# Optimization experiments

Measured on AMD Instinct MI355X. Metric: run time of the kernel, lower is better.

The kernel has to match this reference:

```python
import jax, jax.numpy as jnp
import numpy as np

COMMITMENT_WEIGHT = 0.25


def setup_inputs() -> dict:
    key = jax.random.key(0)
    k1, k2 = jax.random.split(key)
    z = jax.random.normal(k1, (16, 512, 2048), dtype=jnp.float32)
    codebooks = jax.random.normal(k2, (8, 1024, 512), dtype=jnp.float32) * 0.01
    return {"z": z, "codebooks": codebooks}


def reference(z, codebooks):
    """Residual VQ forward (eval mode, no EMA update).
    z: [B, D, T], codebooks: [Q, N, D].
    Returns (quantized [B, D, T], codes [B, Q, T], total_loss scalar).
    """
    B, D, T = z.shape
    Q = codebooks.shape[0]
    zt = jnp.transpose(z, (0, 2, 1))  # [B, T, D]

    residual = zt
    quantized = jnp.zeros_like(zt)
    codes = []
    total_loss = jnp.float32(0.0)
    for q in range(Q):
        cb = codebooks[q]  # [N, D]
        # squared euclidean distances (argmin-equivalent to cdist)
        d2 = (jnp.sum(residual * residual, axis=-1, keepdims=True)
              - 2.0 * jnp.einsum('btd,nd->btn', residual, cb)
              + jnp.sum(cb * cb, axis=-1))  # [B, T, N]
        idx = jnp.argmin(d2, axis=-1)  # [B, T]
        codes.append(idx)
        q_step = cb[idx]  # [B, T, D] embedding gather
        quantized = quantized + q_step
        commit = jnp.mean((jax.lax.stop_gradient(residual) - q_step) ** 2)
        commit = jnp.clip(commit, 0.0, 10.0)
        total_loss = total_loss + commit * COMMITMENT_WEIGHT
        residual = residual - jax.lax.stop_gradient(q_step)

    total_loss = jnp.clip(total_loss, 0.0, 10.0)
    q_bdt = jnp.transpose(quantized, (0, 2, 1))  # [B, D, T]
    # faithful to original: raw reshape of [B,T,D] -> [B,D,T] (not a transpose)
    z_res = zt.reshape(B, D, T)
    out = z_res + jax.lax.stop_gradient(q_bdt - z_res)  # straight-through
    codes = jnp.stack(codes, axis=1)  # [B, Q, T]
    return out, codes, total_loss
```

## Files before the change

### kernel.cpp

```cpp
#include <hip/hip_runtime.h>
#include <cfloat>

#define BB 16
#define DD 512
#define TT 2048
#define QQ 8
#define NN 1024
#define MM 16
#define RS 520

__device__ __forceinline__ float np_block128_sq(const float* a) {
    float r[8];
    #pragma unroll
    for (int j = 0; j < 8; ++j) r[j] = __fmul_rn(a[j], a[j]);
    #pragma unroll
    for (int i = 8; i < 128; i += 8)
        #pragma unroll
        for (int j = 0; j < 8; ++j) r[j] = __fadd_rn(r[j], __fmul_rn(a[i + j], a[i + j]));
    return __fadd_rn(__fadd_rn(__fadd_rn(r[0], r[1]), __fadd_rn(r[2], r[3])),
                     __fadd_rn(__fadd_rn(r[4], r[5]), __fadd_rn(r[6], r[7])));
}
__device__ __forceinline__ float np_sum_sq_512(const float* p) {
    const float b0 = np_block128_sq(p);
    const float b1 = np_block128_sq(p + 128);
    const float b2 = np_block128_sq(p + 256);
    const float b3 = np_block128_sq(p + 384);
    return __fadd_rn(__fadd_rn(b0, b1), __fadd_rn(b2, b3));
}

__global__ __launch_bounds__(64) void rvq_init(double* lossws) {
    if (threadIdx.x < QQ) lossws[threadIdx.x] = 0.0;
}

__global__ __launch_bounds__(256) void rvq_cnorm(const float* __restrict__ cbs,
                                                 float* __restrict__ cnorm) {
    const int gid = blockIdx.x * 256 + threadIdx.x;
    cnorm[gid] = np_sum_sq_512(cbs + (size_t)gid * DD);
}

__global__ __launch_bounds__(256) void rvq_argmin(const float* __restrict__ z,
                                                  const float* __restrict__ cbs,
                                                  const float* __restrict__ cnorm,
                                                  int* __restrict__ codes_ws) {
    __shared__ float resid[MM * RS];
    __shared__ float A_sh[MM];
    __shared__ int   sel[MM];
    __shared__ float redv[MM * 128];
    __shared__ int   redi[MM * 128];

    const int tid = threadIdx.x;
    const int blk = blockIdx.x;
    const int b   = blk >> 7;
    const int t0  = (blk & 127) * MM;
    const float* zb = z + (size_t)b * DD * TT + t0;

    for (int p = 0; p < 32; ++p) {
        const int d = (tid >> 4) + p * 16;
        const int m = tid & 15;
        resid[m * RS + d] = zb[(size_t)d * TT + m];
    }
    __syncthreads();
    if (tid < MM) A_sh[tid] = np_sum_sq_512(resid + tid * RS);

    const int half  = tid >> 7;
    const int nl    = tid & 127;
    const int mbase = half * 8;

    for (int q = 0; q < QQ; ++q) {
        __syncthreads();
        const float* cbq = cbs + (size_t)q * NN * DD;

        float bv[8]; int bi[8];
        #pragma unroll
        for (int i = 0; i < 8; ++i) { bv[i] = FLT_MAX; bi[i] = 0; }

        for (int nb = 0; nb < 2; ++nb) {
            const int n0 = nb * 512 + nl;
            const float* c0 = cbq + (size_t)(n0      ) * DD;
            const float* c1 = cbq + (size_t)(n0 + 128) * DD;
            const float* c2 = cbq + (size_t)(n0 + 256) * DD;
            const float* c3 = cbq + (size_t)(n0 + 384) * DD;

            float4 acc[8][4];
            #pragma unroll
            for (int m = 0; m < 8; ++m)
                #pragma unroll
                for (int j = 0; j < 4; ++j) acc[m][j] = make_float4(0.f, 0.f, 0.f, 0.f);

            const float* rb = resid + mbase * RS;

            for (int k8 = 0; k8 < 64; ++k8) {
                const int ko = k8 * 8;
                const float4 w0a = *(const float4*)(c0 + ko), w0b = *(const float4*)(c0 + ko + 4);
                const float4 w1a = *(const float4*)(c1 + ko), w1b = *(const float4*)(c1 + ko + 4);
                const float4 w2a = *(const float4*)(c2 + ko), w2b = *(const float4*)(c2 + ko + 4);
                const float4 w3a = *(const float4*)(c3 + ko), w3b = *(const float4*)(c3 + ko + 4);
                #pragma unroll
                for (int m = 0; m < 8; ++m) {
                    const float4 r0 = *(const float4*)(rb + m * RS + ko);
                    const float4 r1 = *(const float4*)(rb + m * RS + ko + 4);
                    acc[m][0].x = __fadd_rn(acc[m][0].x, __fmul_rn(r0.x, w0a.x));
                    acc[m][0].y = __fadd_rn(acc[m][0].y, __fmul_rn(r0.y, w0a.y));
                    acc[m][0].z = __fadd_rn(acc[m][0].z, __fmul_rn(r0.z, w0a.z));
                    acc[m][0].w = __fadd_rn(acc[m][0].w, __fmul_rn(r0.w, w0a.w));
                    acc[m][0].x = __fadd_rn(acc[m][0].x, __fmul_rn(r1.x, w0b.x));
                    acc[m][0].y = __fadd_rn(acc[m][0].y, __fmul_rn(r1.y, w0b.y));
                    acc[m][0].z = __fadd_rn(acc[m][0].z, __fmul_rn(r1.z, w0b.z));
                    acc[m][0].w = __fadd_rn(acc[m][0].w, __fmul_rn(r1.w, w0b.w));
                    acc[m][1].x = __fadd_rn(acc[m][1].x, __fmul_rn(r0.x, w1a.x));
                    acc[m][1].y = __fadd_rn(acc[m][1].y, __fmul_rn(r0.y, w1a.y));
                    acc[m][1].z = __fadd_rn(acc[m][1].z, __fmul_rn(r0.z, w1a.z));
                    acc[m][1].w = __fadd_rn(acc[m][1].w, __fmul_rn(r0.w, w1a.w));
                    acc[m][1].x = __fadd_rn(acc[m][1].x, __fmul_rn(r1.x, w1b.x));
                    acc[m][1].y = __fadd_rn(acc[m][1].y, __fmul_rn(r1.y, w1b.y));
                    acc[m][1].z = __fadd_rn(acc[m][1].z, __fmul_rn(r1.z, w1b.z));
                    acc[m][1].w = __fadd_rn(acc[m][1].w, __fmul_rn(r1.w, w1b.w));
                    acc[m][2].x = __fadd_rn(acc[m][2].x, __fmul_rn(r0.x, w2a.x));
                    acc[m][2].y = __fadd_rn(acc[m][2].y, __fmul_rn(r0.y, w2a.y));
                    acc[m][2].z = __fadd_rn(acc[m][2].z, __fmul_rn(r0.z, w2a.z));
                    acc[m][2].w = __fadd_rn(acc[m][2].w, __fmul_rn(r0.w, w2a.w));
                    acc[m][2].x = __fadd_rn(acc[m][2].x, __fmul_rn(r1.x, w2b.x));
                    acc[m][2].y = __fadd_rn(acc[m][2].y, __fmul_rn(r1.y, w2b.y));
                    acc[m][2].z = __fadd_rn(acc[m][2].z, __fmul_rn(r1.z, w2b.z));
                    acc[m][2].w = __fadd_rn(acc[m][2].w, __fmul_rn(r1.w, w2b.w));
                    acc[m][3].x = __fadd_rn(acc[m][3].x, __fmul_rn(r0.x, w3a.x));
                    acc[m][3].y = __fadd_rn(acc[m][3].y, __fmul_rn(r0.y, w3a.y));
                    acc[m][3].z = __fadd_rn(acc[m][3].z, __fmul_rn(r0.z, w3a.z));
                    acc[m][3].w = __fadd_rn(acc[m][3].w, __fmul_rn(r0.w, w3a.w));
                    acc[m][3].x = __fadd_rn(acc[m][3].x, __fmul_rn(r1.x, w3b.x));
                    acc[m][3].y = __fadd_rn(acc[m][3].y, __fmul_rn(r1.y, w3b.y));
                    acc[m][3].z = __fadd_rn(acc[m][3].z, __fmul_rn(r1.z, w3b.z));
                    acc[m][3].w = __fadd_rn(acc[m][3].w, __fmul_rn(r1.w, w3b.w));
                }
            }
            #pragma unroll
            for (int j = 0; j < 4; ++j) {
                const int n = n0 + j * 128;
                const float Cn = cnorm[q * NN + n];
                #pragma unroll
                for (int m = 0; m < 8; ++m) {
                    const float4 a = acc[m][j];
                    const float E = __fadd_rn(__fadd_rn(a.x, a.z), __fadd_rn(a.y, a.w));
                    const float s = __fadd_rn(__fsub_rn(A_sh[mbase + m], __fmul_rn(2.0f, E)), Cn);
                    if (s < bv[m]) { bv[m] = s; bi[m] = n; }
                }
            }
        }

        __syncthreads();
        #pragma unroll
        for (int m = 0; m < 8; ++m) {
            redv[(mbase + m) * 128 + nl] = bv[m];
            redi[(mbase + m) * 128 + nl] = bi[m];
        }
        __syncthreads();
        {
            const int m = tid >> 4, j0 = tid & 15;
            float v  = redv[m * 128 + j0];
            int   ix = redi[m * 128 + j0];
            for (int u = 1; u < 8; ++u) {
                const float v2 = redv[m * 128 + j0 + 16 * u];
                const int   i2 = redi[m * 128 + j0 + 16 * u];
                if (v2 < v || (v2 == v && i2 < ix)) { v = v2; ix = i2; }
            }
            #pragma unroll
            for (int mask = 1; mask < 16; mask <<= 1) {
                const float v2 = __shfl_xor(v, mask, 64);
                const int   i2 = __shfl_xor(ix, mask, 64);
                if (v2 < v || (v2 == v && i2 < ix)) { v = v2; ix = i2; }
            }
            if (j0 == 0) {
                sel[m] = ix;
                codes_ws[b * QQ * TT + q * TT + t0 + m] = ix;
            }
        }
        __syncthreads();

        if (q < QQ - 1) {
            const int m = tid >> 4, l16 = tid & 15;
            const float* cr = cbq + (size_t)sel[m] * DD;
            for (int jj = 0; jj < 32; ++jj) {
                const int d = l16 + jj * 16;
                resid[m * RS + d] = __fsub_rn(resid[m * RS + d], cr[d]);
            }
            __syncthreads();
            if (tid < MM) A_sh[tid] = np_sum_sq_512(resid + tid * RS);
        }
    }
}

__global__ __launch_bounds__(256) void rvq_build(const float* __restrict__ z,
                                                 const float* __restrict__ cbs,
                                                 const int* __restrict__ codes_ws,
                                                 float* __restrict__ out,
                                                 double* __restrict__ lossws) {
    __shared__ int    lcode[MM * QQ];
    __shared__ double lpart[4][QQ];

    const int tid = threadIdx.x;
    const int blk = blockIdx.x;
    const int b   = blk >> 7;
    const int t0  = (blk & 127) * MM;

    if (tid < MM * QQ) {
        const int m = tid >> 3;
        const int q = tid & 7;
        const int c = codes_ws[b * QQ * TT + q * TT + t0 + m];
        lcode[tid] = c;
        out[(size_t)BB * DD * TT + (size_t)b * QQ * TT + (size_t)q * TT + t0 + m] = (float)c;
    }
    __syncthreads();

    const int m  = tid & 15;
    const int dl = tid >> 4;

    double lsum[QQ];
    #pragma unroll
    for (int q = 0; q < QQ; ++q) lsum[q] = 0.0;

    for (int p = 0; p < DD / 16; ++p) {
        const int d = dl + p * 16;
        float r  = z[(size_t)b * DD * TT + (size_t)d * TT + t0 + m];
        float qa = 0.0f;
        #pragma unroll
        for (int q = 0; q < QQ; ++q) {
            const float c = cbs[(size_t)q * NN * DD + (size_t)lcode[m * 8 + q] * DD + d];
            qa = __fadd_rn(qa, c);
            r  = __fsub_rn(r, c);
            lsum[q] += (double)r * (double)r;
        }
        out[(size_t)b * DD * TT + (size_t)d * TT + t0 + m] = qa;
    }

    const int wid = tid >> 6, lane = tid & 63;
    #pragma unroll
    for (int q = 0; q < QQ; ++q) {
        double v = lsum[q];
        #pragma unroll
        for (int off = 32; off > 0; off >>= 1) v += __shfl_down(v, off, 64);
        lsum[q] = v;
    }
    if (lane == 0) {
        #pragma unroll
        for (int q = 0; q < QQ; ++q) lpart[wid][q] = lsum[q];
    }
    __syncthreads();
    if (tid < QQ) {
        const double s = lpart[0][tid] + lpart[1][tid] + lpart[2][tid] + lpart[3][tid];
        atomicAdd(&lossws[tid], s);
    }
}

__global__ __launch_bounds__(64) void rvq_final(const double* __restrict__ lossws,
                                                float* __restrict__ out) {
    if (threadIdx.x == 0) {
        double tot = 0.0;
        for (int q = 0; q < QQ; ++q) {
            double c = lossws[q] / (double)((size_t)BB * TT * DD);
            c = c < 0.0 ? 0.0 : (c > 10.0 ? 10.0 : c);
            tot += 0.25 * c;
        }
        tot = tot < 0.0 ? 0.0 : (tot > 10.0 ? 10.0 : tot);
        out[(size_t)BB * DD * TT + (size_t)BB * QQ * TT] = (float)tot;
    }
}

extern "C" void kernel_launch(void* const* d_in, const int* in_sizes, int n_in,
                              void* d_out, int out_size, void* d_ws, size_t ws_size,
                              hipStream_t stream) {
    const float* z   = (const float*)d_in[0];
    const float* cbs = (const float*)d_in[1];
    float* out       = (float*)d_out;
    double* lossws   = (double*)d_ws;
    float* cnorm     = (float*)((char*)d_ws + 64);
    int* codes_ws    = (int*)((char*)d_ws + 64 + QQ * NN * 4);

    rvq_init  <<<1, 64, 0, stream>>>(lossws);
    rvq_cnorm <<<QQ * NN / 256, 256, 0, stream>>>(cbs, cnorm);
    rvq_argmin<<<BB * (TT / MM), 256, 0, stream>>>(z, cbs, cnorm, codes_ws);
    rvq_build <<<BB * (TT / MM), 256, 0, stream>>>(z, cbs, codes_ws, out, lossws);
    rvq_final <<<1, 64, 0, stream>>>(lossws, out);
}
```

Baseline: 8.717 ms.

## Use FMA-contracted distance pass with exact rescoring of near-minimum candidates

The main codebook-distance loop now uses plain multiply-adds the compiler may fuse into FMAs, instead of separate correctly-rounded multiply and add. Each thread keeps its top-two candidates, and the block finds the approximate minimum per row. Candidates within a small margin are then rescored with the original strict arithmetic, and the winner is picked with a packed 64-bit atomicMin. The accumulator tile is halved and launch bounds now request 4 blocks, to cut register pressure and raise occupancy. The risk is that the margin may miss the true argmin when FMA rounding moves a score by more than that margin, and the rescoring adds serial per-thread dot products.

```diff
diff --git a/kernel.cpp b/kernel.cpp
--- a/kernel.cpp
+++ b/kernel.cpp
@@ -8,6 +8,7 @@
 #define NN 1024
 #define MM 16
 #define RS 520
+#define MARGIN 1e-3f
 
 __device__ __forceinline__ float np_block128_sq(const float* a) {
     float r[8];
@@ -27,6 +28,20 @@
     const float b3 = np_block128_sq(p + 384);
     return __fadd_rn(__fadd_rn(b0, b1), __fadd_rn(b2, b3));
 }
+__device__ __forceinline__ float np_dot_512(const float* r, const float* w) {
+    float a0 = 0.f, a1 = 0.f, a2 = 0.f, a3 = 0.f;
+    for (int ko = 0; ko < 512; ko += 8) {
+        a0 = __fadd_rn(a0, __fmul_rn(r[ko + 0], w[ko + 0]));
+        a1 = __fadd_rn(a1, __fmul_rn(r[ko + 1], w[ko + 1]));
+        a2 = __fadd_rn(a2, __fmul_rn(r[ko + 2], w[ko + 2]));
+        a3 = __fadd_rn(a3, __fmul_rn(r[ko + 3], w[ko + 3]));
+        a0 = __fadd_rn(a0, __fmul_rn(r[ko + 4], w[ko + 4]));
+        a1 = __fadd_rn(a1, __fmul_rn(r[ko + 5], w[ko + 5]));
+        a2 = __fadd_rn(a2, __fmul_rn(r[ko + 6], w[ko + 6]));
+        a3 = __fadd_rn(a3, __fmul_rn(r[ko + 7], w[ko + 7]));
+    }
+    return __fadd_rn(__fadd_rn(a0, a2), __fadd_rn(a1, a3));
+}
 
 __global__ __launch_bounds__(64) void rvq_init(double* lossws) {
     if (threadIdx.x < QQ) lossws[threadIdx.x] = 0.0;
@@ -38,15 +53,16 @@
     cnorm[gid] = np_sum_sq_512(cbs + (size_t)gid * DD);
 }
 
-__global__ __launch_bounds__(256) void rvq_argmin(const float* __restrict__ z,
-                                                  const float* __restrict__ cbs,
-                                                  const float* __restrict__ cnorm,
-                                                  int* __restrict__ codes_ws) {
+__global__ __launch_bounds__(256, 4) void rvq_argmin(const float* __restrict__ z,
+                                                     const float* __restrict__ cbs,
+                                                     const float* __restrict__ cnorm,
+                                                     int* __restrict__ codes_ws) {
     __shared__ float resid[MM * RS];
     __shared__ float A_sh[MM];
     __shared__ int   sel[MM];
-    __shared__ float redv[MM * 128];
-    __shared__ int   redi[MM * 128];
+    __shared__ float wmin[4][8];
+    __shared__ float amin_sh[MM];
+    __shared__ unsigned long long cand_sh[MM];
 
     const int tid = threadIdx.x;
     const int blk = blockIdx.x;
@@ -65,114 +81,122 @@
     const int half  = tid >> 7;
     const int nl    = tid & 127;
     const int mbase = half * 8;
+    const int wv    = tid >> 6;
+    const float* rb = resid + mbase * RS;
 
     for (int q = 0; q < QQ; ++q) {
         __syncthreads();
         const float* cbq = cbs + (size_t)q * NN * DD;
 
-        float bv[8]; int bi[8];
-        #pragma unroll
-        for (int i = 0; i < 8; ++i) { bv[i] = FLT_MAX; bi[i] = 0; }
-
-        for (int nb = 0; nb < 2; ++nb) {
-            const int n0 = nb * 512 + nl;
-            const float* c0 = cbq + (size_t)(n0      ) * DD;
-            const float* c1 = cbq + (size_t)(n0 + 128) * DD;
-            const float* c2 = cbq + (size_t)(n0 + 256) * DD;
-            const float* c3 = cbq + (size_t)(n0 + 384) * DD;
-
-            float4 acc[8][4];
+        float Af[8];
+        #pragma unroll
+        for (int mm = 0; mm < 8; ++mm) Af[mm] = A_sh[mbase + mm];
+
+        float v1[8], v2[8]; int n1[8], n2[8];
+        #pragma unroll
+        for (int mm = 0; mm < 8; ++mm) { v1[mm] = FLT_MAX; v2[mm] = FLT_MAX; n1[mm] = 0; n2[mm] = 0; }
+
+        for (int ch = 0; ch < 4; ++ch) {
+            const int na = ch * 256 + nl;
+            const int nb2 = na + 128;
+            const float* cA = cbq + (size_t)na * DD;
+            const float* cB = cbq + (size_t)nb2 * DD;
+
+            float4 acc[8][2];
             #pragma unroll
-            for (int m = 0; m < 8; ++m)
-                #pragma unroll
-                for (int j = 0; j < 4; ++j) acc[m][j] = make_float4(0.f, 0.f, 0.f, 0.f);
-
-            const float* rb = resid + mbase * RS;
-
+            for (int mm = 0; mm < 8; ++mm) {
+                acc[mm][0] = make_float4(0.f, 0.f, 0.f, 0.f);
+                acc[mm][1] = make_float4(0.f, 0.f, 0.f, 0.f);
+            }
+
+            #pragma unroll 2
             for (int k8 = 0; k8 < 64; ++k8) {
                 const int ko = k8 * 8;
-                const float4 w0a = *(const float4*)(c0 + ko), w0b = *(const float4*)(c0 + ko + 4);
-                const float4 w1a = *(const float4*)(c1 + ko), w1b = *(const float4*)(c1 + ko + 4);
-                const float4 w2a = *(const float4*)(c2 + ko), w2b = *(const float4*)(c2 + ko + 4);
-                const float4 w3a = *(const float4*)(c3 + ko), w3b = *(const float4*)(c3 + ko + 4);
+                const float4 wa0 = *(const float4*)(cA + ko);
+                const float4 wa1 = *(const float4*)(cA + ko + 4);
+                const float4 wb0 = *(const float4*)(cB + ko);
+                const float4 wb1 = *(const float4*)(cB + ko + 4);
                 #pragma unroll
-                for (int m = 0; m < 8; ++m) {
-                    const float4 r0 = *(const float4*)(rb + m * RS + ko);
-                    const float4 r1 = *(const float4*)(rb + m * RS + ko + 4);
-                    acc[m][0].x = __fadd_rn(acc[m][0].x, __fmul_rn(r0.x, w0a.x));
-                    acc[m][0].y = __fadd_rn(acc[m][0].y, __fmul_rn(r0.y, w0a.y));
-                    acc[m][0].z = __fadd_rn(acc[m][0].z, __fmul_rn(r0.z, w0a.z));
-                    acc[m][0].w = __fadd_rn(acc[m][0].w, __fmul_rn(r0.w, w0a.w));
-                    acc[m][0].x = __fadd_rn(acc[m][0].x, __fmul_rn(r1.x, w0b.x));
-                    acc[m][0].y = __fadd_rn(acc[m][0].y, __fmul_rn(r1.y, w0b.y));
-                    acc[m][0].z = __fadd_rn(acc[m][0].z, __fmul_rn(r1.z, w0b.z));
-                    acc[m][0].w = __fadd_rn(acc[m][0].w, __fmul_rn(r1.w, w0b.w));
-                    acc[m][1].x = __fadd_rn(acc[m][1].x, __fmul_rn(r0.x, w1a.x));
-                    acc[m][1].y = __fadd_rn(acc[m][1].y, __fmul_rn(r0.y, w1a.y));
-                    acc[m][1].z = __fadd_rn(acc[m][1].z, __fmul_rn(r0.z, w1a.z));
-                    acc[m][1].w = __fadd_rn(acc[m][1].w, __fmul_rn(r0.w, w1a.w));
-                    acc[m][1].x = __fadd_rn(acc[m][1].x, __fmul_rn(r1.x, w1b.x));
-                    acc[m][1].y = __fadd_rn(acc[m][1].y, __fmul_rn(r1.y, w1b.y));
-                    acc[m][1].z = __fadd_rn(acc[m][1].z, __fmul_rn(r1.z, w1b.z));
-                    acc[m][1].w = __fadd_rn(acc[m][1].w, __fmul_rn(r1.w, w1b.w));
-                    acc[m][2].x = __fadd_rn(acc[m][2].x, __fmul_rn(r0.x, w2a.x));
-                    acc[m][2].y = __fadd_rn(acc[m][2].y, __fmul_rn(r0.y, w2a.y));
-                    acc[m][2].z = __fadd_rn(acc[m][2].z, __fmul_rn(r0.z, w2a.z));
-                    acc[m][2].w = __fadd_rn(acc[m][2].w, __fmul_rn(r0.w, w2a.w));
-                    acc[m][2].x = __fadd_rn(acc[m][2].x, __fmul_rn(r1.x, w2b.x));
-                    acc[m][2].y = __fadd_rn(acc[m][2].y, __fmul_rn(r1.y, w2b.y));
-                    acc[m][2].z = __fadd_rn(acc[m][2].z, __fmul_rn(r1.z, w2b.z));
-                    acc[m][2].w = __fadd_rn(acc[m][2].w, __fmul_rn(r1.w, w2b.w));
-                    acc[m][3].x = __fadd_rn(acc[m][3].x, __fmul_rn(r0.x, w3a.x));
-                    acc[m][3].y = __fadd_rn(acc[m][3].y, __fmul_rn(r0.y, w3a.y));
-                    acc[m][3].z = __fadd_rn(acc[m][3].z, __fmul_rn(r0.z, w3a.z));
-                    acc[m][3].w = __fadd_rn(acc[m][3].w, __fmul_rn(r0.w, w3a.w));
-                    acc[m][3].x = __fadd_rn(acc[m][3].x, __fmul_rn(r1.x, w3b.x));
-                    acc[m][3].y = __fadd_rn(acc[m][3].y, __fmul_rn(r1.y, w3b.y));
-                    acc[m][3].z = __fadd_rn(acc[m][3].z, __fmul_rn(r1.z, w3b.z));
-                    acc[m][3].w = __fadd_rn(acc[m][3].w, __fmul_rn(r1.w, w3b.w));
+                for (int mm = 0; mm < 8; ++mm) {
+                    const float4 r0 = *(const float4*)(rb + mm * RS + ko);
+                    const float4 r1 = *(const float4*)(rb + mm * RS + ko + 4);
+                    acc[mm][0].x += r0.x * wa0.x; acc[mm][0].y += r0.y * wa0.y;
+                    acc[mm][0].z += r0.z * wa0.z; acc[mm][0].w += r0.w * wa0.w;
+                    acc[mm][0].x += r1.x * wa1.x; acc[mm][0].y += r1.y * wa1.y;
+                    acc[mm][0].z += r1.z * wa1.z; acc[mm][0].w += r1.w * wa1.w;
+                    acc[mm][1].x += r0.x * wb0.x; acc[mm][1].y += r0.y * wb0.y;
+                    acc[mm][1].z += r0.z * wb0.z; acc[mm][1].w += r0.w * wb0.w;
+                    acc[mm][1].x += r1.x * wb1.x; acc[mm][1].y += r1.y * wb1.y;
+                    acc[mm][1].z += r1.z * wb1.z; acc[mm][1].w += r1.w * wb1.w;
                 }
             }
+            const float CnA = cnorm[q * NN + na];
+            const float CnB = cnorm[q * NN + nb2];
             #pragma unroll
-            for (int j = 0; j < 4; ++j) {
-                const int n = n0 + j * 128;
-                const float Cn = cnorm[q * NN + n];
+            for (int mm = 0; mm < 8; ++mm) {
+                const float4 aA = acc[mm][0];
+                const float4 aB = acc[mm][1];
+                const float EA = (aA.x + aA.z) + (aA.y + aA.w);
+                const float EB = (aB.x + aB.z) + (aB.y + aB.w);
+                const float sA = (Af[mm] - 2.0f * EA) + CnA;
+                const float sB = (Af[mm] - 2.0f * EB) + CnB;
+                if (sA < v1[mm])      { v2[mm] = v1[mm]; n2[mm] = n1[mm]; v1[mm] = sA; n1[mm] = na; }
+                else if (sA < v2[mm]) { v2[mm] = sA; n2[mm] = na; }
+                if (sB < v1[mm])      { v2[mm] = v1[mm]; n2[mm] = n1[mm]; v1[mm] = sB; n1[mm] = nb2; }
+                else if (sB < v2[mm]) { v2[mm] = sB; n2[mm] = nb2; }
+            }
+        }
+
+        #pragma unroll
+        for (int mm = 0; mm < 8; ++mm) {
+            float v = v1[mm];
+            #pragma unroll
+            for (int mask = 1; mask < 64; mask <<= 1) {
+                const float o = __shfl_xor(v, mask, 64);
+                v = o < v ? o : v;
+            }
+            if ((tid & 63) == 0) wmin[wv][mm] = v;
+        }
+        __syncthreads();
+        if (tid < MM) {
+            const int h2 = tid >> 3;
+            amin_sh[tid] = fminf(wmin[h2 * 2][tid & 7], wmin[h2 * 2 + 1][tid & 7]);
+            cand_sh[tid] = 0xFFFFFFFFFFFFFFFFull;
+        }
+        __syncthreads();
+
+        #pragma unroll
+        for (int mm = 0; mm < 8; ++mm) {
+            const int mg = mbase + mm;
+            const float thr = amin_sh[mg] + MARGIN;
+            if (v2[mm] <= thr) {
                 #pragma unroll
-                for (int m = 0; m < 8; ++m) {
-                    const float4 a = acc[m][j];
-                    const float E = __fadd_rn(__fadd_rn(a.x, a.z), __fadd_rn(a.y, a.w));
-                    const float s = __fadd_rn(__fsub_rn(A_sh[mbase + m], __fmul_rn(2.0f, E)), Cn);
-                    if (s < bv[m]) { bv[m] = s; bi[m] = n; }
-                }
-            }
-        }
-
-        __syncthreads();
-        #pragma unroll
-        for (int m = 0; m < 8; ++m) {
-            redv[(mbase + m) * 128 + nl] = bv[m];
-            redi[(mbase + m) * 128 + nl] = bi[m];
-        }
-        __syncthreads();
-        {
-            const int m = tid >> 4, j0 = tid & 15;
-            float v  = redv[m * 128 + j0];
-            int   ix = redi[m * 128 + j0];
-            for (int u = 1; u < 8; ++u) {
-                const float v2 = redv[m * 128 + j0 + 16 * u];
-                const int   i2 = redi[m * 128 + j0 + 16 * u];
-                if (v2 < v || (v2 == v && i2 < ix)) { v = v2; ix = i2; }
-            }
-            #pragma unroll
-            for (int mask = 1; mask < 16; mask <<= 1) {
-                const float v2 = __shfl_xor(v, mask, 64);
-                const int   i2 = __shfl_xor(ix, mask, 64);
-                if (v2 < v || (v2 == v && i2 < ix)) { v = v2; ix = i2; }
-            }
-            if (j0 == 0) {
-                sel[m] = ix;
-                codes_ws[b * QQ * TT + q * TT + t0 + m] = ix;
-            }
+                for (int ch = 0; ch < 4; ++ch)
+                    #pragma unroll
+                    for (int cw = 0; cw < 2; ++cw) {
+                        const int n = ch * 256 + cw * 128 + nl;
+                        const float E = np_dot_512(resid + mg * RS, cbq + (size_t)n * DD);
+                        const float s = __fadd_rn(__fsub_rn(Af[mm], __fmul_rn(2.0f, E)),
+                                                  cnorm[q * NN + n]);
+                        const unsigned long long pk =
+                            ((unsigned long long)__float_as_uint(s) << 32) | (unsigned)n;
+                        atomicMin(&cand_sh[mg], pk);
+                    }
+            } else if (v1[mm] <= thr) {
+                const int n = n1[mm];
+                const float E = np_dot_512(resid + mg * RS, cbq + (size_t)n * DD);
+                const float s = __fadd_rn(__fsub_rn(Af[mm], __fmul_rn(2.0f, E)),
+                                          cnorm[q * NN + n]);
+                const unsigned long long pk =
+                    ((unsigned long long)__float_as_uint(s) << 32) | (unsigned)n;
+                atomicMin(&cand_sh[mg], pk);
+            }
+        }
+        __syncthreads();
+        if (tid < MM) {
+            const int ix = (int)(cand_sh[tid] & 0x3FF);
+            sel[tid] = ix;
+            codes_ws[b * QQ * TT + q * TT + t0 + tid] = ix;
         }
         __syncthreads();
 
```

Result: slower. 25.34 ms (+190.8%).
